# Performance work log

Measured on AMD Instinct MI355X. Metric: run time of the kernel, lower is better.

The kernel has to match this reference:

```python
import jax, jax.numpy as jnp
import numpy as np

B, O, H2, L, S = 256, 1024, 2048, 2, 12  # batch, output_dim, 2*hidden_dim, num_layers, enc seq len


def setup_inputs() -> dict:
    key = jax.random.key(0)
    ks = jax.random.split(key, 18)
    def rn(k, shape, scale=1.0):
        return jax.random.normal(k, shape, jnp.float32) * scale
    s = 0.02  # weight scale to keep softmax/gates in a sane range
    return {
        "x": rn(ks[0], (1, B, O)),
        "h0": rn(ks[1], (L, B, H2)),
        "c0": rn(ks[2], (L, B, H2)),
        "encoder_outputs": rn(ks[3], (S, B, H2)),
        "attn_W": rn(ks[4], (S, H2 + O), s), "attn_b": rn(ks[5], (S,), s),
        "comb_W": rn(ks[6], (O, H2 + O), s), "comb_b": rn(ks[7], (O,), s),
        "Wih0": rn(ks[8], (4 * H2, O), s), "Whh0": rn(ks[9], (4 * H2, H2), s),
        "bih0": rn(ks[10], (4 * H2,), s), "bhh0": rn(ks[11], (4 * H2,), s),
        "Wih1": rn(ks[12], (4 * H2, H2), s), "Whh1": rn(ks[13], (4 * H2, H2), s),
        "bih1": rn(ks[14], (4 * H2,), s), "bhh1": rn(ks[15], (4 * H2,), s),
        "out_W": rn(ks[16], (O, H2), s), "out_b": rn(ks[17], (O,), s),
    }


def _lstm_cell(x, h, c, Wih, Whh, bih, bhh):
    # PyTorch LSTM cell: gates in (i, f, g, o) order
    gates = x @ Wih.T + bih + h @ Whh.T + bhh  # [B, 4*H2]
    i, f, g, o = jnp.split(gates, 4, axis=-1)
    c_new = jax.nn.sigmoid(f) * c + jax.nn.sigmoid(i) * jnp.tanh(g)
    h_new = jax.nn.sigmoid(o) * jnp.tanh(c_new)
    return h_new, c_new


def reference(x, h0, c0, encoder_outputs, attn_W, attn_b, comb_W, comb_b,
              Wih0, Whh0, bih0, bhh0, Wih1, Whh1, bih1, bhh1, out_W, out_b):
    x0 = x[0]  # [B, O]
    # Bahdanau-style attention over the 12 encoder steps
    attn_in = jnp.concatenate([x0, h0[0]], axis=1)               # [B, O+2H]
    attn_weights = jax.nn.softmax(attn_in @ attn_W.T + attn_b, axis=1)  # [B, S]
    attn_applied = jnp.einsum('bs,sbh->bh', attn_weights, encoder_outputs)  # [B, 2H]
    # combine + relu
    xc = jnp.concatenate([x0, attn_applied], axis=1)             # [B, O+2H]
    xin = jax.nn.relu(xc @ comb_W.T + comb_b)                    # [B, O]
    # single-step 2-layer LSTM (dropout=0)
    h1, c1 = _lstm_cell(xin, h0[0], c0[0], Wih0, Whh0, bih0, bhh0)
    h2, c2 = _lstm_cell(h1, h0[1], c0[1], Wih1, Whh1, bih1, bhh1)
    output = h2[None]                                            # [1, B, 2H]
    prediction = output @ out_W.T + out_b                        # [1, B, O]
    h_new = jnp.stack([h1, h2], axis=0)
    c_new = jnp.stack([c1, c2], axis=0)
    return prediction, h_new, c_new
```

## Files before the change

kernel.cpp:

```cpp
#include <hip/hip_runtime.h>
#include <hip/hip_bf16.h>

typedef short short8 __attribute__((ext_vector_type(8)));
typedef short short4v __attribute__((ext_vector_type(4)));
typedef float floatx4 __attribute__((ext_vector_type(4)));

#define BB 256
#define OO 1024
#define HH 2048
#define SS 12
#define LSTRIDE 72

__device__ __forceinline__ __hip_bfloat16 f2b(float x) { return __float2bfloat16(x); }
__device__ __forceinline__ float sigf(float x) { return 1.0f / (1.0f + expf(-x)); }

__device__ __forceinline__ short8 cvt8v(float4 lo, float4 hi) {
    union { short8 s; __hip_bfloat16 h[8]; } u;
    u.h[0] = f2b(lo.x); u.h[1] = f2b(lo.y); u.h[2] = f2b(lo.z); u.h[3] = f2b(lo.w);
    u.h[4] = f2b(hi.x); u.h[5] = f2b(hi.y); u.h[6] = f2b(hi.z); u.h[7] = f2b(hi.w);
    return u.s;
}
__device__ __forceinline__ short4v cvt4v(float4 v) {
    union { short4v s; __hip_bfloat16 h[4]; } u;
    u.h[0] = f2b(v.x); u.h[1] = f2b(v.y); u.h[2] = f2b(v.z); u.h[3] = f2b(v.w);
    return u.s;
}

__global__ __launch_bounds__(256)
void attn_logits(const float* __restrict__ x0,
                 const float* __restrict__ h00,
                 const float* __restrict__ attn_W,
                 const float* __restrict__ attn_b,
                 float* __restrict__ wts)
{
    const int b = blockIdx.x;
    const int tid = threadIdx.x;
    const int lane = tid & 63;
    const int wave = tid >> 6;

    float part[SS];
#pragma unroll
    for (int s = 0; s < SS; s++) part[s] = 0.f;

#pragma unroll
    for (int k = 0; k < 3; k++) {
        const int c = tid + (k << 8);
        float4 v = (k == 0) ? *(const float4*)(x0 + (size_t)b * OO + (c << 2))
                            : *(const float4*)(h00 + (size_t)b * HH + ((c - 256) << 2));
#pragma unroll
        for (int s = 0; s < SS; s++) {
            float4 w4 = *(const float4*)(attn_W + (size_t)s * (OO + HH) + (c << 2));
            part[s] += v.x * w4.x + v.y * w4.y + v.z * w4.z + v.w * w4.w;
        }
    }
#pragma unroll
    for (int s = 0; s < SS; s++) {
#pragma unroll
        for (int off = 32; off > 0; off >>= 1)
            part[s] += __shfl_down(part[s], off);
    }
    __shared__ float red[4][SS];
    if (lane == 0) {
#pragma unroll
        for (int s = 0; s < SS; s++) red[wave][s] = part[s];
    }
    __syncthreads();
    if (tid == 0) {
        float logits[SS];
        float mx = -1e30f;
        for (int s = 0; s < SS; s++) {
            logits[s] = red[0][s] + red[1][s] + red[2][s] + red[3][s] + attn_b[s];
            mx = fmaxf(mx, logits[s]);
        }
        float sum = 0.f;
        for (int s = 0; s < SS; s++) { logits[s] = expf(logits[s] - mx); sum += logits[s]; }
        float inv = 1.0f / sum;
        for (int s = 0; s < SS; s++) wts[b * SS + s] = logits[s] * inv;
    }
}

__global__ __launch_bounds__(256)
void attn_apply(const float* __restrict__ enc,
                const float* __restrict__ wts,
                float* __restrict__ attn_out)
{
    const int b = blockIdx.x >> 1;
    const int half = blockIdx.x & 1;
    const int tid = threadIdx.x;
    __shared__ float w[SS];
    if (tid < SS) w[tid] = wts[b * SS + tid];
    __syncthreads();
    const int h = (half << 10) + (tid << 2);
    float4 a = {0.f, 0.f, 0.f, 0.f};
#pragma unroll
    for (int s = 0; s < SS; s++) {
        float4 e = *(const float4*)(enc + ((size_t)(s * BB + b) * HH) + h);
        float ws = w[s];
        a.x += ws * e.x; a.y += ws * e.y; a.z += ws * e.z; a.w += ws * e.w;
    }
    *(float4*)(attn_out + (size_t)b * HH + h) = a;
}

template<int K1, int K2, bool RELU>
__global__ __launch_bounds__(256)
void gemm_dual(const float* __restrict__ A1,
               const float* __restrict__ W1, int ldw1, int ofs1,
               const float* __restrict__ A2,
               const float* __restrict__ W2, int ldw2, int ofs2,
               const float* __restrict__ bias1,
               const float* __restrict__ bias2,
               float* __restrict__ Cout, int ldc)
{
    constexpr int n1 = K1 >> 6;
    constexpr int nT = (K1 + K2) >> 6;
    __shared__ __attribute__((aligned(16))) __hip_bfloat16 As[2][16][LSTRIDE];
    __shared__ __attribute__((aligned(16))) __hip_bfloat16 Ws[2][32][LSTRIDE];
    __shared__ float red[2][16][17];
    const int tid = threadIdx.x;
    const int lane = tid & 63;
    const int wave = tid >> 6;
    const int quad = lane >> 4, l15 = lane & 15;
    const int cf = wave & 1;
    const int kh = wave >> 1;
    const int m_base = blockIdx.y * 16;
    const int n_base = blockIdx.x * 32;

    const int arow = tid >> 4, acol = (tid & 15) << 2;
    const int wrow = tid >> 3, wcol = (tid & 7) << 3;

    const float* baseA1 = A1 + (size_t)(m_base + arow) * K1 + acol;
    const float* baseA2 = A2 + (size_t)(m_base + arow) * K2 + acol;
    const float* baseW1 = W1 + (size_t)(n_base + wrow) * ldw1 + ofs1 + wcol;
    const float* baseW2 = W2 + (size_t)(n_base + wrow) * ldw2 + ofs2 + wcol;

    float4 pa, pw0, pw1;
    auto issue = [&](int tt) {
        const float *ap, *wp;
        if (tt < n1) { ap = baseA1 + (tt << 6);        wp = baseW1 + (tt << 6); }
        else         { ap = baseA2 + ((tt - n1) << 6); wp = baseW2 + ((tt - n1) << 6); }
        pa  = *(const float4*)(ap);
        pw0 = *(const float4*)(wp);
        pw1 = *(const float4*)(wp + 4);
    };
    issue(0);

    floatx4 acc = (floatx4){0.f, 0.f, 0.f, 0.f};
    for (int t = 0; t < nT; t++) {
        const int buf = t & 1;
        *(short4v*)(&As[buf][arow][acol]) = cvt4v(pa);
        *(short8*)(&Ws[buf][wrow][wcol])  = cvt8v(pw0, pw1);
        __syncthreads();
        if (t + 1 < nT) issue(t + 1);
        short8 af = *(const short8*)(&As[buf][l15][kh * 32 + quad * 8]);
        short8 bf = *(const short8*)(&Ws[buf][cf * 16 + l15][kh * 32 + quad * 8]);
        acc = __builtin_amdgcn_mfma_f32_16x16x32_bf16(af, bf, acc, 0, 0, 0);
    }

    if (kh == 1) {
#pragma unroll
        for (int r = 0; r < 4; r++) red[cf][l15][quad * 4 + r] = acc[r];
    }
    __syncthreads();
    if (kh == 0) {
        const int col = n_base + cf * 16 + l15;
        float bsum = bias1[col] + (bias2 ? bias2[col] : 0.f);
#pragma unroll
        for (int r = 0; r < 4; r++) {
            const int row = m_base + quad * 4 + r;
            float v = acc[r] + red[cf][l15][quad * 4 + r] + bsum;
            if (RELU) v = fmaxf(v, 0.f);
            Cout[(size_t)row * ldc + col] = v;
        }
    }
}

#define A_BUF_BYTES 16384
#define W_BUF_BYTES 8192
__device__ __forceinline__ int swzA(int buf, int row, int c8) {
    return (buf << 14) + ((((row << 6) | (c8 << 4))) ^ ((row & 7) << 4));
}
__device__ __forceinline__ int swzW(int buf, int row, int c8) {
    return 2 * A_BUF_BYTES + (buf << 13) + ((((row << 6) | (c8 << 4))) ^ ((row & 7) << 4));
}

template<int K1>
__global__ __launch_bounds__(512)
void lstm_gates(const float* __restrict__ A1,
                const float* __restrict__ Wih,
                const float* __restrict__ A2,
                const float* __restrict__ Whh,
                float* __restrict__ P)
{
    constexpr int KTOT = K1 + HH;
    constexpr int KPER = KTOT / 4;
    constexpr int NT = KPER / 32;
    __shared__ __attribute__((aligned(128))) unsigned char lds[2 * A_BUF_BYTES + 2 * W_BUF_BYTES];

    const int tid = threadIdx.x;
    const int lane = tid & 63;
    const int wave = tid >> 6;
    const int quad = lane >> 4, l15 = lane & 15;

    const int L    = blockIdx.x + (blockIdx.y << 6);
    const int xcd  = L & 7;
    const int slot = L >> 3;
    const int ks   = xcd >> 1;
    const int nb   = ((xcd & 1) << 5) | slot;
    const int n_base = nb << 5;
    const int k0 = ks * KPER;

    const int arow = tid >> 1;
    const int ac8  = (tid & 1) << 1;
    const int wrow = tid >> 2;
    const int wc8  = tid & 3;
    const int grow = (wrow >> 5) * HH + n_base + (wrow & 31);

    const float* bA1 = A1 + (size_t)arow * K1 + (ac8 << 3);
    const float* bA2 = A2 + (size_t)arow * HH + (ac8 << 3);
    const float* bW1 = Wih + (size_t)grow * K1 + (wc8 << 3);
    const float* bW2 = Whh + (size_t)grow * HH + (wc8 << 3);

    float4 paA[4], pwA[2], paB[4], pwB[2];
    auto issue = [&](int tt, float4 (&pa)[4], float4 (&pw)[2]) {
        const int gk = k0 + (tt << 5);
        const float *ap, *wp;
        if (gk < K1) { ap = bA1 + gk;        wp = bW1 + gk; }
        else         { ap = bA2 + (gk - K1); wp = bW2 + (gk - K1); }
#pragma unroll
        for (int j = 0; j < 4; j++) pa[j] = *(const float4*)(ap + (j << 2));
#pragma unroll
        for (int j = 0; j < 2; j++) pw[j] = *(const float4*)(wp + (j << 2));
    };
    issue(0, paA, pwA);
    issue(1, paB, pwB);

    floatx4 acc[2][4][2];
#pragma unroll
    for (int mf = 0; mf < 2; mf++)
#pragma unroll
        for (int g = 0; g < 4; g++)
#pragma unroll
            for (int nf = 0; nf < 2; nf++)
                acc[mf][g][nf] = (floatx4){0.f, 0.f, 0.f, 0.f};

    auto store_tile = [&](int buf, float4 (&pa)[4], float4 (&pw)[2]) {
        *(short8*)(lds + swzA(buf, arow, ac8))     = cvt8v(pa[0], pa[1]);
        *(short8*)(lds + swzA(buf, arow, ac8 | 1)) = cvt8v(pa[2], pa[3]);
        *(short8*)(lds + swzW(buf, wrow, wc8))     = cvt8v(pw[0], pw[1]);
    };
    auto compute = [&](int buf) {
        short8 af[2];
#pragma unroll
        for (int mf = 0; mf < 2; mf++)
            af[mf] = *(const short8*)(lds + swzA(buf, (wave << 5) + (mf << 4) + l15, quad));
#pragma unroll
        for (int g = 0; g < 4; g++)
#pragma unroll
            for (int nf = 0; nf < 2; nf++) {
                short8 bf = *(const short8*)(lds + swzW(buf, (g << 5) + (nf << 4) + l15, quad));
                acc[0][g][nf] = __builtin_amdgcn_mfma_f32_16x16x32_bf16(af[0], bf, acc[0][g][nf], 0, 0, 0);
                acc[1][g][nf] = __builtin_amdgcn_mfma_f32_16x16x32_bf16(af[1], bf, acc[1][g][nf], 0, 0, 0);
            }
    };

    for (int t = 0; t < NT; t += 2) {
        store_tile(0, paA, pwA);
        if (t + 2 < NT) issue(t + 2, paA, pwA);
        __syncthreads();
        compute(0);
        store_tile(1, paB, pwB);
        if (t + 3 < NT) issue(t + 3, paB, pwB);
        __syncthreads();
        compute(1);
    }

    float* Pk = P + (size_t)ks * (256 * 8192);
#pragma unroll
    for (int mf = 0; mf < 2; mf++)
#pragma unroll
        for (int g = 0; g < 4; g++)
#pragma unroll
            for (int nf = 0; nf < 2; nf++) {
                const int col = n_base + (nf << 4) + l15;
#pragma unroll
                for (int r = 0; r < 4; r++) {
                    const int row = (wave << 5) + (mf << 4) + (quad << 2) + r;
                    Pk[(size_t)row * 8192 + g * HH + col] = acc[mf][g][nf][r];
                }
            }
}

__global__ __launch_bounds__(512)
void lstm_cell(const float* __restrict__ P,
               const float* __restrict__ bih,
               const float* __restrict__ bhh,
               const float* __restrict__ c0,
               float* __restrict__ h_out,
               float* __restrict__ c_out)
{
    const int gid = blockIdx.x * 512 + threadIdx.x;
    const int row = gid >> 9;
    const int col = (gid & 511) << 2;

    float4 gate[4];
#pragma unroll
    for (int g = 0; g < 4; g++) {
        const size_t base = (size_t)row * 8192 + g * HH + col;
        float4 s = *(const float4*)(P + base);
#pragma unroll
        for (int k = 1; k < 4; k++) {
            float4 v = *(const float4*)(P + (size_t)k * (256 * 8192) + base);
            s.x += v.x; s.y += v.y; s.z += v.z; s.w += v.w;
        }
        float4 b1 = *(const float4*)(bih + g * HH + col);
        float4 b2 = *(const float4*)(bhh + g * HH + col);
        s.x += b1.x + b2.x; s.y += b1.y + b2.y; s.z += b1.z + b2.z; s.w += b1.w + b2.w;
        gate[g] = s;
    }
    const size_t idx = (size_t)row * HH + col;
    float4 cv = *(const float4*)(c0 + idx);
    float4 hn, cn;
    {
        float c_ = sigf(gate[1].x) * cv.x + sigf(gate[0].x) * tanhf(gate[2].x);
        cn.x = c_; hn.x = sigf(gate[3].x) * tanhf(c_);
        c_ = sigf(gate[1].y) * cv.y + sigf(gate[0].y) * tanhf(gate[2].y);
        cn.y = c_; hn.y = sigf(gate[3].y) * tanhf(c_);
        c_ = sigf(gate[1].z) * cv.z + sigf(gate[0].z) * tanhf(gate[2].z);
        cn.z = c_; hn.z = sigf(gate[3].z) * tanhf(c_);
        c_ = sigf(gate[1].w) * cv.w + sigf(gate[0].w) * tanhf(gate[2].w);
        cn.w = c_; hn.w = sigf(gate[3].w) * tanhf(c_);
    }
    *(float4*)(h_out + idx) = hn;
    *(float4*)(c_out + idx) = cn;
}

extern "C" void kernel_launch(void* const* d_in, const int* in_sizes, int n_in,
                              void* d_out, int out_size, void* d_ws, size_t ws_size,
                              hipStream_t stream) {
    const float* x      = (const float*)d_in[0];
    const float* h0     = (const float*)d_in[1];
    const float* c0     = (const float*)d_in[2];
    const float* enc    = (const float*)d_in[3];
    const float* attn_W = (const float*)d_in[4];
    const float* attn_b = (const float*)d_in[5];
    const float* comb_W = (const float*)d_in[6];
    const float* comb_b = (const float*)d_in[7];
    const float* Wih0   = (const float*)d_in[8];
    const float* Whh0   = (const float*)d_in[9];
    const float* bih0   = (const float*)d_in[10];
    const float* bhh0   = (const float*)d_in[11];
    const float* Wih1   = (const float*)d_in[12];
    const float* Whh1   = (const float*)d_in[13];
    const float* bih1   = (const float*)d_in[14];
    const float* bhh1   = (const float*)d_in[15];
    const float* out_W  = (const float*)d_in[16];
    const float* out_b  = (const float*)d_in[17];

    float* pred = (float*)d_out;
    float* h1   = pred + 262144;
    float* h2   = h1 + 524288;
    float* c1   = h2 + 524288;
    float* c2   = c1 + 524288;
    const float* h0_l0 = h0;
    const float* h0_l1 = h0 + 524288;
    const float* c0_l0 = c0;
    const float* c0_l1 = c0 + 524288;

    float* xin      = pred;
    float* attn_out = c2;
    float* wts      = c1;
    float* P        = (float*)d_ws;

    attn_logits<<<dim3(BB), dim3(256), 0, stream>>>(x, h0_l0, attn_W, attn_b, wts);

    attn_apply<<<dim3(BB * 2), dim3(256), 0, stream>>>(enc, wts, attn_out);

    gemm_dual<OO, HH, true><<<dim3(OO / 32, BB / 16), dim3(256), 0, stream>>>(
        x, comb_W, OO + HH, 0,
        attn_out, comb_W, OO + HH, OO,
        comb_b, nullptr, xin, OO);

    lstm_gates<OO><<<dim3(64, 4), dim3(512), 0, stream>>>(xin, Wih0, h0_l0, Whh0, P);
    lstm_cell<<<dim3(256), dim3(512), 0, stream>>>(P, bih0, bhh0, c0_l0, h1, c1);

    lstm_gates<HH><<<dim3(64, 4), dim3(512), 0, stream>>>(h1, Wih1, h0_l1, Whh1, P);
    lstm_cell<<<dim3(256), dim3(512), 0, stream>>>(P, bih1, bhh1, c0_l1, h2, c2);

    gemm_dual<HH, 0, false><<<dim3(OO / 32, BB / 16), dim3(256), 0, stream>>>(
        h2, out_W, HH, 0,
        h2, out_W, HH, 0,
        out_b, nullptr, pred, OO);
}
```

Measured before the change: 398.8 us.

## Fuse attention kernels, retile LSTM gate GEMM, split-K small GEMMs with epilogue

```diff
diff --git a/kernel.cpp b/kernel.cpp
--- a/kernel.cpp
+++ b/kernel.cpp
@@ -9,7 +9,6 @@
 #define OO 1024
 #define HH 2048
 #define SS 12
-#define LSTRIDE 72
 
 __device__ __forceinline__ __hip_bfloat16 f2b(float x) { return __float2bfloat16(x); }
 __device__ __forceinline__ float sigf(float x) { return 1.0f / (1.0f + expf(-x)); }
@@ -26,12 +25,20 @@
     return u.s;
 }
 
-__global__ __launch_bounds__(256)
-void attn_logits(const float* __restrict__ x0,
-                 const float* __restrict__ h00,
-                 const float* __restrict__ attn_W,
-                 const float* __restrict__ attn_b,
-                 float* __restrict__ wts)
+__device__ __forceinline__ int swz16(int row, int c16) {
+    return ((row << 6) | (c16 << 4)) ^ ((row & 7) << 4);
+}
+__device__ __forceinline__ int swz8(int row, int c8) {
+    return ((row << 6) | (c8 << 3)) ^ ((row & 7) << 4);
+}
+
+__global__ __launch_bounds__(512)
+void attn_fused(const float* __restrict__ x0,
+                const float* __restrict__ h00,
+                const float* __restrict__ enc,
+                const float* __restrict__ attn_W,
+                const float* __restrict__ attn_b,
+                float* __restrict__ attn_out)
 {
     const int b = blockIdx.x;
     const int tid = threadIdx.x;
@@ -42,14 +49,20 @@
 #pragma unroll
     for (int s = 0; s < SS; s++) part[s] = 0.f;
 
-#pragma unroll
-    for (int k = 0; k < 3; k++) {
-        const int c = tid + (k << 8);
-        float4 v = (k == 0) ? *(const float4*)(x0 + (size_t)b * OO + (c << 2))
-                            : *(const float4*)(h00 + (size_t)b * HH + ((c - 256) << 2));
+    {
+        float4 v = (tid < 256) ? *(const float4*)(x0 + (size_t)b * OO + (tid << 2))
+                               : *(const float4*)(h00 + (size_t)b * HH + ((tid - 256) << 2));
 #pragma unroll
         for (int s = 0; s < SS; s++) {
-            float4 w4 = *(const float4*)(attn_W + (size_t)s * (OO + HH) + (c << 2));
+            float4 w4 = *(const float4*)(attn_W + (size_t)s * (OO + HH) + (tid << 2));
+            part[s] += v.x * w4.x + v.y * w4.y + v.z * w4.z + v.w * w4.w;
+        }
+    }
+    if (tid < 256) {
+        float4 v = *(const float4*)(h00 + (size_t)b * HH + ((tid + 256) << 2));
+#pragma unroll
+        for (int s = 0; s < SS; s++) {
+            float4 w4 = *(const float4*)(attn_W + (size_t)s * (OO + HH) + ((tid + 512) << 2));
             part[s] += v.x * w4.x + v.y * w4.y + v.z * w4.z + v.w * w4.w;
         }
     }
@@ -59,7 +72,8 @@
         for (int off = 32; off > 0; off >>= 1)
             part[s] += __shfl_down(part[s], off);
     }
-    __shared__ float red[4][SS];
+    __shared__ float red[8][SS];
+    __shared__ float sw[SS];
     if (lane == 0) {
 #pragma unroll
         for (int s = 0; s < SS; s++) red[wave][s] = part[s];
@@ -69,118 +83,26 @@
         float logits[SS];
         float mx = -1e30f;
         for (int s = 0; s < SS; s++) {
-            logits[s] = red[0][s] + red[1][s] + red[2][s] + red[3][s] + attn_b[s];
-            mx = fmaxf(mx, logits[s]);
+            float v = attn_b[s];
+            for (int w = 0; w < 8; w++) v += red[w][s];
+            logits[s] = v;
+            mx = fmaxf(mx, v);
         }
         float sum = 0.f;
         for (int s = 0; s < SS; s++) { logits[s] = expf(logits[s] - mx); sum += logits[s]; }
         float inv = 1.0f / sum;
-        for (int s = 0; s < SS; s++) wts[b * SS + s] = logits[s] * inv;
-    }
-}
-
-__global__ __launch_bounds__(256)
-void attn_apply(const float* __restrict__ enc,
-                const float* __restrict__ wts,
-                float* __restrict__ attn_out)
-{
-    const int b = blockIdx.x >> 1;
-    const int half = blockIdx.x & 1;
-    const int tid = threadIdx.x;
-    __shared__ float w[SS];
-    if (tid < SS) w[tid] = wts[b * SS + tid];
+        for (int s = 0; s < SS; s++) sw[s] = logits[s] * inv;
+    }
     __syncthreads();
-    const int h = (half << 10) + (tid << 2);
+
     float4 a = {0.f, 0.f, 0.f, 0.f};
 #pragma unroll
     for (int s = 0; s < SS; s++) {
-        float4 e = *(const float4*)(enc + ((size_t)(s * BB + b) * HH) + h);
-        float ws = w[s];
+        float4 e = *(const float4*)(enc + ((size_t)(s * BB + b) * HH) + (tid << 2));
+        float ws = sw[s];
         a.x += ws * e.x; a.y += ws * e.y; a.z += ws * e.z; a.w += ws * e.w;
     }
-    *(float4*)(attn_out + (size_t)b * HH + h) = a;
-}
-
-template<int K1, int K2, bool RELU>
-__global__ __launch_bounds__(256)
-void gemm_dual(const float* __restrict__ A1,
-               const float* __restrict__ W1, int ldw1, int ofs1,
-               const float* __restrict__ A2,
-               const float* __restrict__ W2, int ldw2, int ofs2,
-               const float* __restrict__ bias1,
-               const float* __restrict__ bias2,
-               float* __restrict__ Cout, int ldc)
-{
-    constexpr int n1 = K1 >> 6;
-    constexpr int nT = (K1 + K2) >> 6;
-    __shared__ __attribute__((aligned(16))) __hip_bfloat16 As[2][16][LSTRIDE];
-    __shared__ __attribute__((aligned(16))) __hip_bfloat16 Ws[2][32][LSTRIDE];
-    __shared__ float red[2][16][17];
-    const int tid = threadIdx.x;
-    const int lane = tid & 63;
-    const int wave = tid >> 6;
-    const int quad = lane >> 4, l15 = lane & 15;
-    const int cf = wave & 1;
-    const int kh = wave >> 1;
-    const int m_base = blockIdx.y * 16;
-    const int n_base = blockIdx.x * 32;
-
-    const int arow = tid >> 4, acol = (tid & 15) << 2;
-    const int wrow = tid >> 3, wcol = (tid & 7) << 3;
-
-    const float* baseA1 = A1 + (size_t)(m_base + arow) * K1 + acol;
-    const float* baseA2 = A2 + (size_t)(m_base + arow) * K2 + acol;
-    const float* baseW1 = W1 + (size_t)(n_base + wrow) * ldw1 + ofs1 + wcol;
-    const float* baseW2 = W2 + (size_t)(n_base + wrow) * ldw2 + ofs2 + wcol;
-
-    float4 pa, pw0, pw1;
-    auto issue = [&](int tt) {
-        const float *ap, *wp;
-        if (tt < n1) { ap = baseA1 + (tt << 6);        wp = baseW1 + (tt << 6); }
-        else         { ap = baseA2 + ((tt - n1) << 6); wp = baseW2 + ((tt - n1) << 6); }
-        pa  = *(const float4*)(ap);
-        pw0 = *(const float4*)(wp);
-        pw1 = *(const float4*)(wp + 4);
-    };
-    issue(0);
-
-    floatx4 acc = (floatx4){0.f, 0.f, 0.f, 0.f};
-    for (int t = 0; t < nT; t++) {
-        const int buf = t & 1;
-        *(short4v*)(&As[buf][arow][acol]) = cvt4v(pa);
-        *(short8*)(&Ws[buf][wrow][wcol])  = cvt8v(pw0, pw1);
-        __syncthreads();
-        if (t + 1 < nT) issue(t + 1);
-        short8 af = *(const short8*)(&As[buf][l15][kh * 32 + quad * 8]);
-        short8 bf = *(const short8*)(&Ws[buf][cf * 16 + l15][kh * 32 + quad * 8]);
-        acc = __builtin_amdgcn_mfma_f32_16x16x32_bf16(af, bf, acc, 0, 0, 0);
-    }
-
-    if (kh == 1) {
-#pragma unroll
-        for (int r = 0; r < 4; r++) red[cf][l15][quad * 4 + r] = acc[r];
-    }
-    __syncthreads();
-    if (kh == 0) {
-        const int col = n_base + cf * 16 + l15;
-        float bsum = bias1[col] + (bias2 ? bias2[col] : 0.f);
-#pragma unroll
-        for (int r = 0; r < 4; r++) {
-            const int row = m_base + quad * 4 + r;
-            float v = acc[r] + red[cf][l15][quad * 4 + r] + bsum;
-            if (RELU) v = fmaxf(v, 0.f);
-            Cout[(size_t)row * ldc + col] = v;
-        }
-    }
-}
-
-#define A_BUF_BYTES 16384
-#define W_BUF_BYTES 8192
-__device__ __forceinline__ int swzA(int buf, int row, int c8) {
-    return (buf << 14) + ((((row << 6) | (c8 << 4))) ^ ((row & 7) << 4));
-}
-__device__ __forceinline__ int swzW(int buf, int row, int c8) {
-    return 2 * A_BUF_BYTES + (buf << 13) + ((((row << 6) | (c8 << 4))) ^ ((row & 7) << 4));
+    *(float4*)(attn_out + (size_t)b * HH + (tid << 2)) = a;
 }
 
 template<int K1>
@@ -194,12 +116,14 @@
     constexpr int KTOT = K1 + HH;
     constexpr int KPER = KTOT / 4;
     constexpr int NT = KPER / 32;
-    __shared__ __attribute__((aligned(128))) unsigned char lds[2 * A_BUF_BYTES + 2 * W_BUF_BYTES];
+    __shared__ __attribute__((aligned(128))) unsigned char lds[49152];
 
     const int tid = threadIdx.x;
     const int lane = tid & 63;
     const int wave = tid >> 6;
     const int quad = lane >> 4, l15 = lane & 15;
+    const int mi = wave >> 1;
+    const int ni = wave & 1;
 
     const int L    = blockIdx.x + (blockIdx.y << 6);
     const int xcd  = L & 7;
@@ -209,58 +133,69 @@
     const int n_base = nb << 5;
     const int k0 = ks * KPER;
 
-    const int arow = tid >> 1;
-    const int ac8  = (tid & 1) << 1;
-    const int wrow = tid >> 2;
-    const int wc8  = tid & 3;
-    const int grow = (wrow >> 5) * HH + n_base + (wrow & 31);
-
-    const float* bA1 = A1 + (size_t)arow * K1 + (ac8 << 3);
-    const float* bA2 = A2 + (size_t)arow * HH + (ac8 << 3);
-    const float* bW1 = Wih + (size_t)grow * K1 + (wc8 << 3);
-    const float* bW2 = Whh + (size_t)grow * HH + (wc8 << 3);
+    const int sr = tid >> 3;
+    const int sc = tid & 7;
+
+    const float* bA1 = A1 + (size_t)sr * K1 + (sc << 2);
+    const float* bA2 = A2 + (size_t)sr * HH + (sc << 2);
+    const int gr0 = (sr >> 5) * HH + n_base + (sr & 31);
+    const int gr1 = ((sr + 64) >> 5) * HH + n_base + ((sr + 64) & 31);
+    const float* bW1_0 = Wih + (size_t)gr0 * K1 + (sc << 2);
+    const float* bW1_1 = Wih + (size_t)gr1 * K1 + (sc << 2);
+    const float* bW2_0 = Whh + (size_t)gr0 * HH + (sc << 2);
+    const float* bW2_1 = Whh + (size_t)gr1 * HH + (sc << 2);
 
     float4 paA[4], pwA[2], paB[4], pwB[2];
     auto issue = [&](int tt, float4 (&pa)[4], float4 (&pw)[2]) {
         const int gk = k0 + (tt << 5);
-        const float *ap, *wp;
-        if (gk < K1) { ap = bA1 + gk;        wp = bW1 + gk; }
-        else         { ap = bA2 + (gk - K1); wp = bW2 + (gk - K1); }
-#pragma unroll
-        for (int j = 0; j < 4; j++) pa[j] = *(const float4*)(ap + (j << 2));
-#pragma unroll
-        for (int j = 0; j < 2; j++) pw[j] = *(const float4*)(wp + (j << 2));
+        if (gk < K1) {
+#pragma unroll
+            for (int j = 0; j < 4; j++)
+                pa[j] = *(const float4*)(bA1 + (size_t)(j << 6) * K1 + gk);
+            pw[0] = *(const float4*)(bW1_0 + gk);
+            pw[1] = *(const float4*)(bW1_1 + gk);
+        } else {
+            const int g2 = gk - K1;
+#pragma unroll
+            for (int j = 0; j < 4; j++)
+                pa[j] = *(const float4*)(bA2 + (size_t)(j << 6) * HH + g2);
+            pw[0] = *(const float4*)(bW2_0 + g2);
+            pw[1] = *(const float4*)(bW2_1 + g2);
+        }
     };
     issue(0, paA, pwA);
     issue(1, paB, pwB);
 
-    floatx4 acc[2][4][2];
-#pragma unroll
-    for (int mf = 0; mf < 2; mf++)
-#pragma unroll
-        for (int g = 0; g < 4; g++)
-#pragma unroll
-            for (int nf = 0; nf < 2; nf++)
-                acc[mf][g][nf] = (floatx4){0.f, 0.f, 0.f, 0.f};
-
-    auto store_tile = [&](int buf, float4 (&pa)[4], float4 (&pw)[2]) {
-        *(short8*)(lds + swzA(buf, arow, ac8))     = cvt8v(pa[0], pa[1]);
-        *(short8*)(lds + swzA(buf, arow, ac8 | 1)) = cvt8v(pa[2], pa[3]);
-        *(short8*)(lds + swzW(buf, wrow, wc8))     = cvt8v(pw[0], pw[1]);
-    };
-    auto compute = [&](int buf) {
-        short8 af[2];
-#pragma unroll
-        for (int mf = 0; mf < 2; mf++)
-            af[mf] = *(const short8*)(lds + swzA(buf, (wave << 5) + (mf << 4) + l15, quad));
-#pragma unroll
-        for (int g = 0; g < 4; g++)
-#pragma unroll
-            for (int nf = 0; nf < 2; nf++) {
-                short8 bf = *(const short8*)(lds + swzW(buf, (g << 5) + (nf << 4) + l15, quad));
-                acc[0][g][nf] = __builtin_amdgcn_mfma_f32_16x16x32_bf16(af[0], bf, acc[0][g][nf], 0, 0, 0);
-                acc[1][g][nf] = __builtin_amdgcn_mfma_f32_16x16x32_bf16(af[1], bf, acc[1][g][nf], 0, 0, 0);
-            }
+    floatx4 acc[4][4];
+#pragma unroll
+    for (int m = 0; m < 4; m++)
+#pragma unroll
+        for (int f = 0; f < 4; f++) acc[m][f] = (floatx4){0.f, 0.f, 0.f, 0.f};
+
+    auto store_tile = [&](int half, float4 (&pa)[4], float4 (&pw)[2]) {
+        unsigned char* Ab = lds + (half << 14);
+        unsigned char* Wb = lds + 32768 + (half << 13);
+#pragma unroll
+        for (int j = 0; j < 4; j++)
+            *(short4v*)(Ab + swz8(sr + (j << 6), sc)) = cvt4v(pa[j]);
+        *(short4v*)(Wb + swz8(sr, sc))      = cvt4v(pw[0]);
+        *(short4v*)(Wb + swz8(sr + 64, sc)) = cvt4v(pw[1]);
+    };
+    auto compute = [&](int half) {
+        const unsigned char* Ab = lds + (half << 14);
+        const unsigned char* Wb = lds + 32768 + (half << 13);
+        short8 af[4], bf[4];
+#pragma unroll
+        for (int m = 0; m < 4; m++)
+            af[m] = *(const short8*)(Ab + swz16((mi << 6) + (m << 4) + l15, quad));
+#pragma unroll
+        for (int f = 0; f < 4; f++)
+            bf[f] = *(const short8*)(Wb + swz16((ni << 6) + (f << 4) + l15, quad));
+#pragma unroll
+        for (int m = 0; m < 4; m++)
+#pragma unroll
+            for (int f = 0; f < 4; f++)
+                acc[m][f] = __builtin_amdgcn_mfma_f32_16x16x32_bf16(af[m], bf[f], acc[m][f], 0, 0, 0);
     };
 
     for (int t = 0; t < NT; t += 2) {
@@ -276,18 +211,139 @@
 
     float* Pk = P + (size_t)ks * (256 * 8192);
 #pragma unroll
-    for (int mf = 0; mf < 2; mf++)
-#pragma unroll
-        for (int g = 0; g < 4; g++)
-#pragma unroll
-            for (int nf = 0; nf < 2; nf++) {
-                const int col = n_base + (nf << 4) + l15;
-#pragma unroll
-                for (int r = 0; r < 4; r++) {
-                    const int row = (wave << 5) + (mf << 4) + (quad << 2) + r;
-                    Pk[(size_t)row * 8192 + g * HH + col] = acc[mf][g][nf][r];
-                }
+    for (int m = 0; m < 4; m++)
+#pragma unroll
+        for (int f = 0; f < 4; f++) {
+            const int gate = (ni << 1) + (f >> 1);
+            const int col  = n_base + ((f & 1) << 4) + l15;
+#pragma unroll
+            for (int r = 0; r < 4; r++) {
+                const int row = (mi << 6) + (m << 4) + (quad << 2) + r;
+                Pk[(size_t)row * 8192 + gate * HH + col] = acc[m][f][r];
             }
+        }
+}
+
+template<int K1, int KTOT>
+__global__ __launch_bounds__(512)
+void gemm_part(const float* __restrict__ A1,
+               const float* __restrict__ A2,
+               const float* __restrict__ W,
+               float* __restrict__ P)
+{
+    constexpr int KPER = KTOT / 8;
+    constexpr int NT = KPER / 32;
+    __shared__ __attribute__((aligned(128))) unsigned char lds[36864];
+
+    const int tid = threadIdx.x;
+    const int lane = tid & 63;
+    const int wave = tid >> 6;
+    const int quad = lane >> 4, l15 = lane & 15;
+    const int mi = wave >> 1;
+    const int ni = wave & 1;
+
+    const int L    = blockIdx.x + (blockIdx.y << 5);
+    const int xcd  = L & 7;
+    const int ks   = xcd;
+    const int nb   = L >> 3;
+    const int n_base = nb << 5;
+    const int k0 = ks * KPER;
+
+    const int sr = tid >> 3;
+    const int sc = tid & 7;
+
+    const float* bA1 = A1 + (size_t)sr * K1 + (sc << 2);
+    const float* bA2 = A2 + (size_t)sr * HH + (sc << 2);
+    const float* bW = W + (size_t)(n_base + sr) * KTOT + (sc << 2);
+
+    float4 paA[4], paB[4];
+    float4 pwA, pwB;
+    auto issue = [&](int tt, float4 (&pa)[4], float4& pw) {
+        const int gk = k0 + (tt << 5);
+        if (gk < K1) {
+#pragma unroll
+            for (int j = 0; j < 4; j++)
+                pa[j] = *(const float4*)(bA1 + (size_t)(j << 6) * K1 + gk);
+        } else {
+            const int g2 = gk - K1;
+#pragma unroll
+            for (int j = 0; j < 4; j++)
+                pa[j] = *(const float4*)(bA2 + (size_t)(j << 6) * HH + g2);
+        }
+        if (tid < 256) pw = *(const float4*)(bW + gk);
+    };
+    issue(0, paA, pwA);
+    issue(1, paB, pwB);
+
+    floatx4 acc[4];
+#pragma unroll
+    for (int m = 0; m < 4; m++) acc[m] = (floatx4){0.f, 0.f, 0.f, 0.f};
+
+    auto store_tile = [&](int half, float4 (&pa)[4], float4& pw) {
+        unsigned char* Ab = lds + (half << 14);
+        unsigned char* Wb = lds + 32768 + (half << 11);
+#pragma unroll
+        for (int j = 0; j < 4; j++)
+            *(short4v*)(Ab + swz8(sr + (j << 6), sc)) = cvt4v(pa[j]);
+        if (tid < 256)
+            *(short4v*)(Wb + swz8(sr, sc)) = cvt4v(pw);
+    };
+    auto compute = [&](int half) {
+        const unsigned char* Ab = lds + (half << 14);
+        const unsigned char* Wb = lds + 32768 + (half << 11);
+        short8 bf = *(const short8*)(Wb + swz16((ni << 4) + l15, quad));
+#pragma unroll
+        for (int m = 0; m < 4; m++) {
+            short8 af = *(const short8*)(Ab + swz16((mi << 6) + (m << 4) + l15, quad));
+            acc[m] = __builtin_amdgcn_mfma_f32_16x16x32_bf16(af, bf, acc[m], 0, 0, 0);
+        }
+    };
+
+    for (int t = 0; t < NT; t += 2) {
+        store_tile(0, paA, pwA);
+        if (t + 2 < NT) issue(t + 2, paA, pwA);
+        __syncthreads();
+        compute(0);
+        store_tile(1, paB, pwB);
+        if (t + 3 < NT) issue(t + 3, paB, pwB);
+        __syncthreads();
+        compute(1);
+    }
+
+    float* Pk = P + (size_t)ks * (256 * 1024);
+    const int col = n_base + (ni << 4) + l15;
+#pragma unroll
+    for (int m = 0; m < 4; m++)
+#pragma unroll
+        for (int r = 0; r < 4; r++) {
+            const int row = (mi << 6) + (m << 4) + (quad << 2) + r;
+            Pk[(size_t)row * 1024 + col] = acc[m][r];
+        }
+}
+
+template<bool RELU>
+__global__ __launch_bounds__(256)
+void gemm_epi(const float* __restrict__ P,
+              const float* __restrict__ bias,
+              float* __restrict__ out)
+{
+    const int gid = blockIdx.x * 256 + threadIdx.x;
+    const int row = gid >> 8;
+    const int c4 = (gid & 255) << 2;
+    const size_t base = (size_t)row * 1024 + c4;
+    float4 s = *(const float4*)(P + base);
+#pragma unroll
+    for (int k = 1; k < 8; k++) {
+        float4 v = *(const float4*)(P + (size_t)k * (256 * 1024) + base);
+        s.x += v.x; s.y += v.y; s.z += v.z; s.w += v.w;
+    }
+    float4 b = *(const float4*)(bias + c4);
+    s.x += b.x; s.y += b.y; s.z += b.z; s.w += b.w;
+    if (RELU) {
+        s.x = fmaxf(s.x, 0.f); s.y = fmaxf(s.y, 0.f);
+        s.z = fmaxf(s.z, 0.f); s.w = fmaxf(s.w, 0.f);
+    }
+    *(float4*)(out + base) = s;
 }
 
 __global__ __launch_bounds__(512)
@@ -368,17 +424,13 @@
 
     float* xin      = pred;
     float* attn_out = c2;
-    float* wts      = c1;
     float* P        = (float*)d_ws;
-
-    attn_logits<<<dim3(BB), dim3(256), 0, stream>>>(x, h0_l0, attn_W, attn_b, wts);
-
-    attn_apply<<<dim3(BB * 2), dim3(256), 0, stream>>>(enc, wts, attn_out);
-
-    gemm_dual<OO, HH, true><<<dim3(OO / 32, BB / 16), dim3(256), 0, stream>>>(
-        x, comb_W, OO + HH, 0,
-        attn_out, comb_W, OO + HH, OO,
-        comb_b, nullptr, xin, OO);
+    float* Pg       = (float*)d_ws;
+
+    attn_fused<<<dim3(BB), dim3(512), 0, stream>>>(x, h0_l0, enc, attn_W, attn_b, attn_out);
+
+    gemm_part<OO, OO + HH><<<dim3(32, 8), dim3(512), 0, stream>>>(x, attn_out, comb_W, Pg);
+    gemm_epi<true><<<dim3(256), dim3(256), 0, stream>>>(Pg, comb_b, xin);
 
     lstm_gates<OO><<<dim3(64, 4), dim3(512), 0, stream>>>(xin, Wih0, h0_l0, Whh0, P);
     lstm_cell<<<dim3(256), dim3(512), 0, stream>>>(P, bih0, bhh0, c0_l0, h1, c1);
@@ -386,8 +438,6 @@
     lstm_gates<HH><<<dim3(64, 4), dim3(512), 0, stream>>>(h1, Wih1, h0_l1, Whh1, P);
     lstm_cell<<<dim3(256), dim3(512), 0, stream>>>(P, bih1, bhh1, c0_l1, h2, c2);
 
-    gemm_dual<HH, 0, false><<<dim3(OO / 32, BB / 16), dim3(256), 0, stream>>>(
-        h2, out_W, HH, 0,
-        h2, out_W, HH, 0,
-        out_b, nullptr, pred, OO);
-}
+    gemm_part<HH, HH><<<dim3(32, 8), dim3(512), 0, stream>>>(h2, h2, out_W, Pg);
+    gemm_epi<false><<<dim3(256), dim3(256), 0, stream>>>(Pg, out_b, pred);
+}
```

After: 364.7 us. -8.5%, faster.
